# Kernel tuning notes

Hardware: AMD Instinct MI355X
Metric: run time of the kernel (lower is better)

## Reference

```python
import jax, jax.numpy as jnp
import numpy as np

VOCAB = 100000
D = 128
BATCH = 16384


def setup_inputs() -> dict:
    key = jax.random.key(0)
    k_idx, k_emb, k_T, k_tv, k_w, k_b = jax.random.split(key, 6)
    bound = float(np.sqrt(3.0 / D))  # matches sqrt(3/embed_size) init scale
    indices = jax.random.randint(k_idx, (BATCH,), 0, VOCAB, dtype=jnp.int64)
    w_embed = jax.random.normal(k_emb, (VOCAB, D), dtype=jnp.float32)
    T = jax.random.uniform(k_T, (D, D, D), dtype=jnp.float32, minval=-bound, maxval=bound)
    B = jnp.zeros((D, D), dtype=jnp.float32)
    time_vec = jax.random.uniform(k_tv, (D,), dtype=jnp.float32, minval=-bound, maxval=bound)
    lin_bound = 1.0 / float(np.sqrt(D))  # nn.Linear default init range
    op_w = jax.random.uniform(k_w, (D, D), dtype=jnp.float32, minval=-lin_bound, maxval=lin_bound)
    op_b = jax.random.uniform(k_b, (D,), dtype=jnp.float32, minval=-lin_bound, maxval=lin_bound)
    return {"indices": indices, "w_embed": w_embed, "T": T, "B": B,
            "time_vec": time_vec, "op_w": op_w, "op_b": op_b}


def reference(indices, w_embed, T, B, time_vec, op_w, op_b):
    # embedding lookup: [b, d]
    we = w_embed[indices]
    # trilinear contraction: [b, d] x [d, d, d] -> [b, d, d], plus bias B
    TransW = jnp.einsum('bx,xyz->byz', we, T) + B[None, :, :]
    # reduce last axis with time_vec: [b, d]
    h3 = jnp.einsum('byz,z->by', TransW, time_vec)
    # op_layer (nn.Linear): x @ W^T + b
    return h3 @ op_w.T + op_b
```

## Files before the change

kernel.cpp:

```cpp
#include <hip/hip_runtime.h>

#define D 128
#define BATCH 16384

typedef float f32x4 __attribute__((ext_vector_type(4)));
typedef short bh8 __attribute__((ext_vector_type(8)));

__device__ __forceinline__ unsigned short f2bf(float f) {
    unsigned u = __float_as_uint(f);
    u += 0x7FFFu + ((u >> 16) & 1u);
    return (unsigned short)(u >> 16);
}

__global__ __launch_bounds__(256) void stage1(
    const float* __restrict__ T, const float* __restrict__ Bm,
    const float* __restrict__ tv, float* __restrict__ m)
{
    const int t = threadIdx.x;
    const int lr = t >> 5;
    const int c4 = t & 31;
    const int R = blockIdx.x * 8 + lr;
    const float* src = (R < BATCH) ? (T + (size_t)R * D)
                                   : (Bm + (size_t)(R - BATCH) * D);
    f32x4 v = *(const f32x4*)(src + c4 * 4);
    f32x4 w = *(const f32x4*)(tv + c4 * 4);
    float p = v[0]*w[0] + v[1]*w[1] + v[2]*w[2] + v[3]*w[3];
#pragma unroll
    for (int s = 16; s >= 1; s >>= 1) p += __shfl_xor(p, s, 32);
    if (c4 == 0) m[R] = p;
}

__global__ __launch_bounds__(128) void stage2(
    const float* __restrict__ m, const float* __restrict__ op_w,
    const float* __restrict__ op_b, unsigned short* __restrict__ W2T,
    float* __restrict__ bias2)
{
    __shared__ float wj[D];
    __shared__ float red[D];
    const int j = blockIdx.x;
    const int x = threadIdx.x;
    if (x < D / 4) ((f32x4*)wj)[x] = ((const f32x4*)(op_w + (size_t)j * D))[x];
    __syncthreads();
    const float* mr = m + (size_t)x * D;
    float acc = 0.f;
#pragma unroll
    for (int k = 0; k < D / 4; ++k) {
        f32x4 a = ((const f32x4*)mr)[k];
        f32x4 b = ((const f32x4*)wj)[k];
        acc += a[0]*b[0] + a[1]*b[1] + a[2]*b[2] + a[3]*b[3];
    }
    W2T[(size_t)j * D + x] = f2bf(acc);
    red[x] = m[(size_t)BATCH * 1 * 0 + 16384 + x] * wj[x];
    __syncthreads();
    if (x == 0) {
        float s = 0.f;
        for (int y = 0; y < D; ++y) s += red[y];
        bias2[j] = s + op_b[j];
    }
}

__global__ __launch_bounds__(256) void main_mfma(
    const int* __restrict__ idx, const float* __restrict__ we,
    const unsigned short* __restrict__ W2T, const float* __restrict__ bias2,
    float* __restrict__ out)
{
    const int t = threadIdx.x;
    const int wv = t >> 6;
    const int l = t & 63;
    const int l15 = l & 15, lg = l >> 4;
    const int b0 = (blockIdx.x * 4 + wv) * 16;

    const int g = idx[b0 + l15];
    const float* arow = we + (size_t)g * D;

    f32x4 acc[8];
#pragma unroll
    for (int c = 0; c < 8; ++c) acc[c] = (f32x4){0.f, 0.f, 0.f, 0.f};

#pragma unroll
    for (int s = 0; s < 4; ++s) {
        f32x4 a0 = *(const f32x4*)(arow + s * 32 + lg * 8);
        f32x4 a1 = *(const f32x4*)(arow + s * 32 + lg * 8 + 4);
        bh8 af;
        af[0] = (short)f2bf(a0[0]); af[1] = (short)f2bf(a0[1]);
        af[2] = (short)f2bf(a0[2]); af[3] = (short)f2bf(a0[3]);
        af[4] = (short)f2bf(a1[0]); af[5] = (short)f2bf(a1[1]);
        af[6] = (short)f2bf(a1[2]); af[7] = (short)f2bf(a1[3]);
#pragma unroll
        for (int c = 0; c < 8; ++c) {
            bh8 bf = *(const bh8*)(W2T + (size_t)(c * 16 + l15) * D + s * 32 + lg * 8);
            acc[c] = __builtin_amdgcn_mfma_f32_16x16x32_bf16(af, bf, acc[c], 0, 0, 0);
        }
    }

#pragma unroll
    for (int c = 0; c < 8; ++c) {
        float bv = bias2[c * 16 + l15];
#pragma unroll
        for (int r = 0; r < 4; ++r) {
            out[(size_t)(b0 + lg * 4 + r) * D + c * 16 + l15] = acc[c][r] + bv;
        }
    }
}

extern "C" void kernel_launch(void* const* d_in, const int* in_sizes, int n_in,
                              void* d_out, int out_size, void* d_ws, size_t ws_size,
                              hipStream_t stream) {
    const int*   idx     = (const int*)d_in[0];
    const float* w_embed = (const float*)d_in[1];
    const float* T       = (const float*)d_in[2];
    const float* Bm      = (const float*)d_in[3];
    const float* tv      = (const float*)d_in[4];
    const float* op_w    = (const float*)d_in[5];
    const float* op_b    = (const float*)d_in[6];
    float* out = (float*)d_out;

    float* m = (float*)d_ws;
    unsigned short* W2T = (unsigned short*)((char*)d_ws + 66048);
    float* bias2 = (float*)((char*)d_ws + 66048 + 32768);

    stage1<<<(BATCH + D + 7) / 8, 256, 0, stream>>>(T, Bm, tv, m);
    stage2<<<D, D, 0, stream>>>(m, op_w, op_b, W2T, bias2);
    main_mfma<<<BATCH / 64, 256, 0, stream>>>(idx, w_embed, W2T, bias2, out);
}
```

Baseline: 22.38 us.

## Fuse weight-prep stages into one kernel and split output columns across waves

Merges the two preprocessing kernels into a single prep kernel, launched with one block per slice of T plus one for B. Each block stages its 128x128 slab in padded shared memory, reduces it against time_vec, then multiplies by op_w, so the m intermediate never goes to global memory and one launch is removed. The main MFMA kernel now handles 16 batch rows per 128-thread block, with each wave covering 64 output columns. All A and B fragments are loaded up front before the MFMAs run. The trade-off is more blocks, and each wave re-reads the gathered embedding rows, in exchange for more parallelism and earlier loads.

```diff
diff --git a/kernel.cpp b/kernel.cpp
--- a/kernel.cpp
+++ b/kernel.cpp
@@ -2,6 +2,7 @@
 
 #define D 128
 #define BATCH 16384
+#define PITCH 132
 
 typedef float f32x4 __attribute__((ext_vector_type(4)));
 typedef short bh8 __attribute__((ext_vector_type(8)));
@@ -12,54 +13,64 @@
     return (unsigned short)(u >> 16);
 }
 
-__global__ __launch_bounds__(256) void stage1(
+__global__ __launch_bounds__(256) void prep(
     const float* __restrict__ T, const float* __restrict__ Bm,
-    const float* __restrict__ tv, float* __restrict__ m)
-{
-    const int t = threadIdx.x;
-    const int lr = t >> 5;
-    const int c4 = t & 31;
-    const int R = blockIdx.x * 8 + lr;
-    const float* src = (R < BATCH) ? (T + (size_t)R * D)
-                                   : (Bm + (size_t)(R - BATCH) * D);
-    f32x4 v = *(const f32x4*)(src + c4 * 4);
-    f32x4 w = *(const f32x4*)(tv + c4 * 4);
-    float p = v[0]*w[0] + v[1]*w[1] + v[2]*w[2] + v[3]*w[3];
-#pragma unroll
-    for (int s = 16; s >= 1; s >>= 1) p += __shfl_xor(p, s, 32);
-    if (c4 == 0) m[R] = p;
-}
-
-__global__ __launch_bounds__(128) void stage2(
-    const float* __restrict__ m, const float* __restrict__ op_w,
+    const float* __restrict__ tv, const float* __restrict__ op_w,
     const float* __restrict__ op_b, unsigned short* __restrict__ W2T,
     float* __restrict__ bias2)
 {
-    __shared__ float wj[D];
-    __shared__ float red[D];
-    const int j = blockIdx.x;
-    const int x = threadIdx.x;
-    if (x < D / 4) ((f32x4*)wj)[x] = ((const f32x4*)(op_w + (size_t)j * D))[x];
+    __shared__ float slab[D * PITCH];
+    __shared__ float m_s[D];
+    const int x = blockIdx.x;
+    const int t = threadIdx.x;
+    const int l = t & 31;
+    const int rg = t >> 5;
+
+    const float* src = (x < D) ? (T + (size_t)x * D * D) : Bm;
+#pragma unroll
+    for (int i = 0; i < 16; ++i) {
+        const int e = i * 1024 + t * 4;
+        const int y = e >> 7, z = e & 127;
+        *(f32x4*)&slab[y * PITCH + z] = *(const f32x4*)(src + e);
+    }
+    const f32x4 tvv = *(const f32x4*)(tv + l * 4);
     __syncthreads();
-    const float* mr = m + (size_t)x * D;
-    float acc = 0.f;
+
 #pragma unroll
-    for (int k = 0; k < D / 4; ++k) {
-        f32x4 a = ((const f32x4*)mr)[k];
-        f32x4 b = ((const f32x4*)wj)[k];
-        acc += a[0]*b[0] + a[1]*b[1] + a[2]*b[2] + a[3]*b[3];
+    for (int yi = 0; yi < 16; ++yi) {
+        const int y = yi * 8 + rg;
+        f32x4 a = *(const f32x4*)&slab[y * PITCH + l * 4];
+        float p = a[0]*tvv[0] + a[1]*tvv[1] + a[2]*tvv[2] + a[3]*tvv[3];
+#pragma unroll
+        for (int s = 16; s >= 1; s >>= 1) p += __shfl_xor(p, s, 32);
+        if (l == 0) m_s[y] = p;
     }
-    W2T[(size_t)j * D + x] = f2bf(acc);
-    red[x] = m[(size_t)BATCH * 1 * 0 + 16384 + x] * wj[x];
     __syncthreads();
-    if (x == 0) {
-        float s = 0.f;
-        for (int y = 0; y < D; ++y) s += red[y];
-        bias2[j] = s + op_b[j];
+
+#pragma unroll
+    for (int i = 0; i < 16; ++i) {
+        const int e = i * 1024 + t * 4;
+        const int y = e >> 7, z = e & 127;
+        *(f32x4*)&slab[y * PITCH + z] = *(const f32x4*)(op_w + e);
+    }
+    __syncthreads();
+
+    const f32x4 mv = *(const f32x4*)&m_s[l * 4];
+#pragma unroll
+    for (int ji = 0; ji < 16; ++ji) {
+        const int j = ji * 8 + rg;
+        f32x4 w = *(const f32x4*)&slab[j * PITCH + l * 4];
+        float p = w[0]*mv[0] + w[1]*mv[1] + w[2]*mv[2] + w[3]*mv[3];
+#pragma unroll
+        for (int s = 16; s >= 1; s >>= 1) p += __shfl_xor(p, s, 32);
+        if (l == 0) {
+            if (x < D) W2T[j * D + x] = f2bf(p);
+            else       bias2[j] = p + op_b[j];
+        }
     }
 }
 
-__global__ __launch_bounds__(256) void main_mfma(
+__global__ __launch_bounds__(128) void main_mfma(
     const int* __restrict__ idx, const float* __restrict__ we,
     const unsigned short* __restrict__ W2T, const float* __restrict__ bias2,
     float* __restrict__ out)
@@ -68,39 +79,52 @@
     const int wv = t >> 6;
     const int l = t & 63;
     const int l15 = l & 15, lg = l >> 4;
-    const int b0 = (blockIdx.x * 4 + wv) * 16;
+    const int b0 = blockIdx.x * 16;
 
     const int g = idx[b0 + l15];
     const float* arow = we + (size_t)g * D;
 
-    f32x4 acc[8];
+    f32x4 a[8];
 #pragma unroll
-    for (int c = 0; c < 8; ++c) acc[c] = (f32x4){0.f, 0.f, 0.f, 0.f};
+    for (int s = 0; s < 4; ++s) {
+        a[2*s]   = *(const f32x4*)(arow + s * 32 + lg * 8);
+        a[2*s+1] = *(const f32x4*)(arow + s * 32 + lg * 8 + 4);
+    }
+    bh8 bfr[4][4];
+#pragma unroll
+    for (int c = 0; c < 4; ++c) {
+        const int j = wv * 64 + c * 16 + l15;
+#pragma unroll
+        for (int s = 0; s < 4; ++s)
+            bfr[c][s] = *(const bh8*)(W2T + (size_t)j * D + s * 32 + lg * 8);
+    }
+    float bias[4];
+#pragma unroll
+    for (int c = 0; c < 4; ++c) bias[c] = bias2[wv * 64 + c * 16 + l15];
+
+    bh8 af[4];
+#pragma unroll
+    for (int s = 0; s < 4; ++s) {
+        af[s][0] = (short)f2bf(a[2*s][0]);   af[s][1] = (short)f2bf(a[2*s][1]);
+        af[s][2] = (short)f2bf(a[2*s][2]);   af[s][3] = (short)f2bf(a[2*s][3]);
+        af[s][4] = (short)f2bf(a[2*s+1][0]); af[s][5] = (short)f2bf(a[2*s+1][1]);
+        af[s][6] = (short)f2bf(a[2*s+1][2]); af[s][7] = (short)f2bf(a[2*s+1][3]);
+    }
+
+    f32x4 acc[4];
+#pragma unroll
+    for (int c = 0; c < 4; ++c) acc[c] = (f32x4){0.f, 0.f, 0.f, 0.f};
+#pragma unroll
+    for (int s = 0; s < 4; ++s)
+#pragma unroll
+        for (int c = 0; c < 4; ++c)
+            acc[c] = __builtin_amdgcn_mfma_f32_16x16x32_bf16(af[s], bfr[c][s], acc[c], 0, 0, 0);
 
 #pragma unroll
-    for (int s = 0; s < 4; ++s) {
-        f32x4 a0 = *(const f32x4*)(arow + s * 32 + lg * 8);
-        f32x4 a1 = *(const f32x4*)(arow + s * 32 + lg * 8 + 4);
-        bh8 af;
-        af[0] = (short)f2bf(a0[0]); af[1] = (short)f2bf(a0[1]);
-        af[2] = (short)f2bf(a0[2]); af[3] = (short)f2bf(a0[3]);
-        af[4] = (short)f2bf(a1[0]); af[5] = (short)f2bf(a1[1]);
-        af[6] = (short)f2bf(a1[2]); af[7] = (short)f2bf(a1[3]);
+    for (int c = 0; c < 4; ++c)
 #pragma unroll
-        for (int c = 0; c < 8; ++c) {
-            bh8 bf = *(const bh8*)(W2T + (size_t)(c * 16 + l15) * D + s * 32 + lg * 8);
-            acc[c] = __builtin_amdgcn_mfma_f32_16x16x32_bf16(af, bf, acc[c], 0, 0, 0);
-        }
-    }
-
-#pragma unroll
-    for (int c = 0; c < 8; ++c) {
-        float bv = bias2[c * 16 + l15];
-#pragma unroll
-        for (int r = 0; r < 4; ++r) {
-            out[(size_t)(b0 + lg * 4 + r) * D + c * 16 + l15] = acc[c][r] + bv;
-        }
-    }
+        for (int r = 0; r < 4; ++r)
+            out[(size_t)(b0 + lg * 4 + r) * D + wv * 64 + c * 16 + l15] = acc[c][r] + bias[c];
 }
 
 extern "C" void kernel_launch(void* const* d_in, const int* in_sizes, int n_in,
@@ -115,11 +139,9 @@
     const float* op_b    = (const float*)d_in[6];
     float* out = (float*)d_out;
 
-    float* m = (float*)d_ws;
-    unsigned short* W2T = (unsigned short*)((char*)d_ws + 66048);
-    float* bias2 = (float*)((char*)d_ws + 66048 + 32768);
+    unsigned short* W2T = (unsigned short*)d_ws;
+    float* bias2 = (float*)((char*)d_ws + 32768);
 
-    stage1<<<(BATCH + D + 7) / 8, 256, 0, stream>>>(T, Bm, tv, m);
-    stage2<<<D, D, 0, stream>>>(m, op_w, op_b, W2T, bias2);
-    main_mfma<<<BATCH / 64, 256, 0, stream>>>(idx, w_embed, W2T, bias2, out);
+    prep<<<D + 1, 256, 0, stream>>>(T, Bm, tv, op_w, op_b, W2T, bias2);
+    main_mfma<<<BATCH / 16, 128, 0, stream>>>(idx, w_embed, W2T, bias2, out);
 }
```

Result: slower. 23.81 us (+6.4%).
